# Performance work log

Hardware: AMD Instinct MI355X
Metric: run time of the kernel (lower is better)

The kernel has to match this reference:

```python
import jax, jax.numpy as jnp
import numpy as np
from jax import lax

IMG_SHAPE = (65, 65, 65)   # X, Y, Z voxels
RESOLUTION = 30.0          # voxel edge length
CENTER = (0.0, 0.0, 0.0)
BANDWIDTH = 10.0           # Gaussian KDE bandwidth
N_POINTS = 2048
CHUNK = 128                # points processed per scan step (N_POINTS % CHUNK == 0)


def _make_target_points():
    # Matches: start = center - res*shape/2; end = start + res*shape; linspace(start, end, shape)
    axes = []
    for c, sh in zip(CENTER, IMG_SHAPE):
        start = c - RESOLUTION * sh / 2.0
        end = start + RESOLUTION * sh
        axes.append(jnp.linspace(start, end, sh, dtype=jnp.float32))
    grid = jnp.meshgrid(*axes, indexing='ij')
    return jnp.stack(grid, axis=0)  # (3, X, Y, Z)


def setup_inputs() -> dict:
    key = jax.random.key(0)
    # Uniform points covering the grid field of view (grid spans roughly +/-975)
    pointcloud = (jax.random.uniform(key, (N_POINTS, 3), dtype=jnp.float32) - 0.5) * 1800.0
    return {"pointcloud": pointcloud, "target_points": _make_target_points()}


def reference(pointcloud, target_points):
    # Gaussian KDE: 1/(2*pi*b^2) * sum_n exp(-||p_n - g||^2 / (2 b^2)) over all voxels g.
    # Same math as the CUDA branch of Voxelise.get_densities, but reduced over N
    # in chunks (online accumulation) instead of materializing (N, 3, X, Y, Z).
    b = jnp.asarray(BANDWIDTH, dtype=pointcloud.dtype)
    inv_norm = 1.0 / (2.0 * jnp.pi * b * b)
    tp = target_points.reshape(3, -1)            # (3, G), G = X*Y*Z
    g = tp.shape[1]
    chunks = pointcloud.reshape(-1, CHUNK, 3)     # (N/CHUNK, CHUNK, 3)

    def body(acc, pc_chunk):
        # (CHUNK, 3, G) diff -> (CHUNK, G) squared distance
        d2 = ((pc_chunk[:, :, None] - tp[None, :, :]) ** 2).sum(axis=1)
        return acc + jnp.exp(-d2 / (2.0 * b * b)).sum(axis=0), None

    acc, _ = lax.scan(body, jnp.zeros((g,), dtype=pointcloud.dtype), chunks)
    return (inv_norm * acc).reshape(IMG_SHAPE)
```

## Files before the change

### kernel.cpp

```cpp
#include <hip/hip_runtime.h>
#include <math.h>


#define NXv   65
#define NYZ   (65 * 65)
#define GTOT  (65 * 65 * 65)
#define TILE  5
#define TILE3 (TILE * TILE * TILE)
#define NT    13
#define TPB   128
#define PMAX  512
#define CUTOFF2 21000.0f

__global__ __launch_bounds__(TPB)
void kde_gather(const float* __restrict__ pc,
                const float* __restrict__ tp,
                float* __restrict__ out,
                int npts) {
    __shared__ float sx[PMAX], sy[PMAX], sz[PMAX];
    __shared__ float axs[3][TILE];
    __shared__ int   cnt;

    const int tid = threadIdx.x;

    const int bt = blockIdx.x;
    const int ti = bt / (NT * NT);
    const int rm = bt - ti * (NT * NT);
    const int tj = rm / NT;
    const int tk = rm - tj * NT;
    const int i0 = ti * TILE, j0 = tj * TILE, k0 = tk * TILE;

    if (tid == 0) cnt = 0;
    if (tid < 3 * TILE) {
        const int axis = tid / TILE;
        const int off  = tid - axis * TILE;
        const int idx  = ((axis == 0) ? i0 : (axis == 1) ? j0 : k0) + off;
        const int strd = (axis == 0) ? NYZ : (axis == 1) ? NXv : 1;
        axs[axis][off] = tp[(size_t)axis * GTOT + (size_t)idx * strd];
    }
    __syncthreads();

    const float xmin = axs[0][0], xmax = axs[0][TILE - 1];
    const float ymin = axs[1][0], ymax = axs[1][TILE - 1];
    const float zmin = axs[2][0], zmax = axs[2][TILE - 1];

    for (int i = tid; i < npts; i += TPB) {
        const float px = pc[3 * i + 0];
        const float py = pc[3 * i + 1];
        const float pz = pc[3 * i + 2];
        const float dx = fmaxf(fmaxf(xmin - px, px - xmax), 0.0f);
        const float dy = fmaxf(fmaxf(ymin - py, py - ymax), 0.0f);
        const float dz = fmaxf(fmaxf(zmin - pz, pz - zmax), 0.0f);
        const float d2 = dx * dx + dy * dy + dz * dz;
        if (d2 < CUTOFF2) {
            const int pos = atomicAdd(&cnt, 1);
            if (pos < PMAX) { sx[pos] = px; sy[pos] = py; sz[pos] = pz; }
        }
    }
    __syncthreads();
    const int np = cnt;

    const float kneg     = (float)(-1.4426950408889634 / 200.0);
    const float inv_norm = 1.0f / (2.0f * 3.14159274101257324f * 100.0f);

    if (tid < TILE3) {
        const int li = tid / (TILE * TILE);
        const int r2 = tid - li * (TILE * TILE);
        const int lj = r2 / TILE;
        const int lk = r2 - lj * TILE;
        const float vx = axs[0][li];
        const float vy = axs[1][lj];
        const float vz = axs[2][lk];
        float acc = 0.0f;
        if (np <= PMAX) {
            #pragma unroll 4
            for (int p = 0; p < np; ++p) {
                const float dx = vx - sx[p];
                const float dy = vy - sy[p];
                const float dz = vz - sz[p];
                const float d2 = fmaf(dx, dx, fmaf(dy, dy, dz * dz));
                acc += exp2f(d2 * kneg);
            }
        } else {
            for (int p = 0; p < npts; ++p) {
                const float dx = vx - pc[3 * p + 0];
                const float dy = vy - pc[3 * p + 1];
                const float dz = vz - pc[3 * p + 2];
                const float d2 = fmaf(dx, dx, fmaf(dy, dy, dz * dz));
                acc += exp2f(d2 * kneg);
            }
        }
        out[(i0 + li) * NYZ + (j0 + lj) * NXv + (k0 + lk)] = acc * inv_norm;
    }
}

extern "C" void kernel_launch(void* const* d_in, const int* in_sizes, int n_in,
                              void* d_out, int out_size, void* d_ws, size_t ws_size,
                              hipStream_t stream) {
    const float* pc  = (const float*)d_in[0];
    const float* tp  = (const float*)d_in[1];
    float*       out = (float*)d_out;

    const int npts = in_sizes[0] / 3;

    kde_gather<<<NT * NT * NT, TPB, 0, stream>>>(pc, tp, out, npts);
}
```

Baseline: 66.33 us.

## Add two-level spatial binning: pre-filter points per supertile before per-tile gather

Adds a first kernel that, for each 2x2x2 supertile of voxel tiles, culls the full point cloud against a cutoff and writes the surviving points to a workspace list. The per-tile kernel then culls only its supertile's list instead of scanning all 2048 points, which cuts the redundant global reads and distance tests done by each of the 2197 blocks. The cost is an extra kernel launch, a serial dependency between the two kernels, and workspace traffic. Tiles whose supertile list overflows fall back to the direct loop over all points.

```diff
diff --git a/kernel.cpp b/kernel.cpp
--- a/kernel.cpp
+++ b/kernel.cpp
@@ -8,27 +8,76 @@
 #define TILE  5
 #define TILE3 (TILE * TILE * TILE)
 #define NT    13
-#define TPB   128
-#define PMAX  512
+#define SG    2
+#define NS    7
+#define NS3   (NS * NS * NS)
+#define CAP   512
+#define TPB_A 256
+#define TPB_B 128
 #define CUTOFF2 21000.0f
 
-__global__ __launch_bounds__(TPB)
-void kde_gather(const float* __restrict__ pc,
-                const float* __restrict__ tp,
-                float* __restrict__ out,
-                int npts) {
-    __shared__ float sx[PMAX], sy[PMAX], sz[PMAX];
+__global__ __launch_bounds__(TPB_A)
+void bin_super(const float* __restrict__ pc,
+               const float* __restrict__ tp,
+               int*   __restrict__ counts,
+               float4* __restrict__ lists,
+               int npts) {
+    __shared__ int cnt;
+    const int b  = blockIdx.x;
+    const int si = b / (NS * NS);
+    const int r  = b - si * (NS * NS);
+    const int sj = r / NS;
+    const int sk = r - sj * NS;
+
+    const int i0 = si * SG * TILE, i1 = min(i0 + SG * TILE - 1, NXv - 1);
+    const int j0 = sj * SG * TILE, j1 = min(j0 + SG * TILE - 1, NXv - 1);
+    const int k0 = sk * SG * TILE, k1 = min(k0 + SG * TILE - 1, NXv - 1);
+
+    const float xmin = tp[(size_t)i0 * NYZ];
+    const float xmax = tp[(size_t)i1 * NYZ];
+    const float ymin = tp[GTOT + (size_t)j0 * NXv];
+    const float ymax = tp[GTOT + (size_t)j1 * NXv];
+    const float zmin = tp[2 * GTOT + k0];
+    const float zmax = tp[2 * GTOT + k1];
+
+    if (threadIdx.x == 0) cnt = 0;
+    __syncthreads();
+
+    for (int i = threadIdx.x; i < npts; i += TPB_A) {
+        const float px = pc[3 * i + 0];
+        const float py = pc[3 * i + 1];
+        const float pz = pc[3 * i + 2];
+        const float dx = fmaxf(fmaxf(xmin - px, px - xmax), 0.0f);
+        const float dy = fmaxf(fmaxf(ymin - py, py - ymax), 0.0f);
+        const float dz = fmaxf(fmaxf(zmin - pz, pz - zmax), 0.0f);
+        if (dx * dx + dy * dy + dz * dz < CUTOFF2) {
+            const int pos = atomicAdd(&cnt, 1);
+            if (pos < CAP) lists[(size_t)b * CAP + pos] = make_float4(px, py, pz, 0.0f);
+        }
+    }
+    __syncthreads();
+    if (threadIdx.x == 0) counts[b] = cnt;
+}
+
+__global__ __launch_bounds__(TPB_B)
+void kde_tile(const float* __restrict__ pc,
+              const float* __restrict__ tp,
+              const int*   __restrict__ counts,
+              const float4* __restrict__ lists,
+              float* __restrict__ out,
+              int npts) {
+    __shared__ float sx[CAP], sy[CAP], sz[CAP];
     __shared__ float axs[3][TILE];
     __shared__ int   cnt;
 
     const int tid = threadIdx.x;
-
-    const int bt = blockIdx.x;
-    const int ti = bt / (NT * NT);
-    const int rm = bt - ti * (NT * NT);
-    const int tj = rm / NT;
-    const int tk = rm - tj * NT;
-    const int i0 = ti * TILE, j0 = tj * TILE, k0 = tk * TILE;
+    const int bt  = blockIdx.x;
+    const int ti  = bt / (NT * NT);
+    const int rm  = bt - ti * (NT * NT);
+    const int tj  = rm / NT;
+    const int tk  = rm - tj * NT;
+    const int i0  = ti * TILE, j0 = tj * TILE, k0 = tk * TILE;
+    const int sb  = (ti / SG) * (NS * NS) + (tj / SG) * NS + (tk / SG);
 
     if (tid == 0) cnt = 0;
     if (tid < 3 * TILE) {
@@ -44,17 +93,19 @@
     const float ymin = axs[1][0], ymax = axs[1][TILE - 1];
     const float zmin = axs[2][0], zmax = axs[2][TILE - 1];
 
-    for (int i = tid; i < npts; i += TPB) {
-        const float px = pc[3 * i + 0];
-        const float py = pc[3 * i + 1];
-        const float pz = pc[3 * i + 2];
-        const float dx = fmaxf(fmaxf(xmin - px, px - xmax), 0.0f);
-        const float dy = fmaxf(fmaxf(ymin - py, py - ymax), 0.0f);
-        const float dz = fmaxf(fmaxf(zmin - pz, pz - zmax), 0.0f);
-        const float d2 = dx * dx + dy * dy + dz * dz;
-        if (d2 < CUTOFF2) {
-            const int pos = atomicAdd(&cnt, 1);
-            if (pos < PMAX) { sx[pos] = px; sy[pos] = py; sz[pos] = pz; }
+    const int  c      = counts[sb];
+    const bool direct = (c > CAP);
+
+    if (!direct) {
+        for (int p = tid; p < c; p += TPB_B) {
+            const float4 q = lists[(size_t)sb * CAP + p];
+            const float dx = fmaxf(fmaxf(xmin - q.x, q.x - xmax), 0.0f);
+            const float dy = fmaxf(fmaxf(ymin - q.y, q.y - ymax), 0.0f);
+            const float dz = fmaxf(fmaxf(zmin - q.z, q.z - zmax), 0.0f);
+            if (dx * dx + dy * dy + dz * dz < CUTOFF2) {
+                const int pos = atomicAdd(&cnt, 1);
+                sx[pos] = q.x; sy[pos] = q.y; sz[pos] = q.z;
+            }
         }
     }
     __syncthreads();
@@ -72,7 +123,7 @@
         const float vy = axs[1][lj];
         const float vz = axs[2][lk];
         float acc = 0.0f;
-        if (np <= PMAX) {
+        if (!direct) {
             #pragma unroll 4
             for (int p = 0; p < np; ++p) {
                 const float dx = vx - sx[p];
@@ -103,5 +154,9 @@
 
     const int npts = in_sizes[0] / 3;
 
-    kde_gather<<<NT * NT * NT, TPB, 0, stream>>>(pc, tp, out, npts);
+    int*    counts = (int*)d_ws;
+    float4* lists  = (float4*)((char*)d_ws + 4096);
+
+    bin_super<<<NS3, TPB_A, 0, stream>>>(pc, tp, counts, lists, npts);
+    kde_tile<<<NT * NT * NT, TPB_B, 0, stream>>>(pc, tp, counts, lists, out, npts);
 }
```

New measurement: 67.63 us. No clear change (+2.0%).
